# Kernel optimization log

Measured on AMD Instinct MI355X. Metric: run time of the kernel, lower is better.

The kernel has to match this reference:

```python
import jax, jax.numpy as jnp
import numpy as np

# ---- column/activation layout (matches transformer_info init kwarg) ----
N_COLS = 20          # continuous data columns
MODES = 50           # VGM modes per column (gumbel-softmax width)
SPAN = MODES + 1     # 1 tanh scalar + MODES gumbel logits
IN_DIM = 2048
OUT_DIM = N_COLS * SPAN  # 1020
TAU = 0.2
B = 16384
EPS = 1e-9

_spans = []
for i in range(N_COLS):
    st = i * SPAN
    _spans.append((st, st + 1, 0))          # tanh span (alpha)
    _spans.append((st + 1, st + SPAN, 1))   # gumbel-softmax span (beta/d)
N_SEG = len(_spans)

_seg = np.zeros(OUT_DIM, np.int32)   # segment id per output feature
_typ = np.zeros(OUT_DIM, np.int32)   # 0 = tanh, 1 = gumbel-softmax
for si, (s, e, t) in enumerate(_spans):
    _seg[s:e] = si
    _typ[s:e] = t
SEG = jnp.asarray(_seg)
TYP = jnp.asarray(_typ)


def setup_inputs() -> dict:
    key = jax.random.key(0)
    kx, kw, kb, ku = jax.random.split(key, 4)
    bound = 1.0 / np.sqrt(IN_DIM)  # init_bounded(dim=input_dim)
    x = jax.random.normal(kx, (B, IN_DIM), dtype=jnp.float32)
    W = jax.random.uniform(kw, (IN_DIM, OUT_DIM), minval=-bound, maxval=bound, dtype=jnp.float32)
    b = jax.random.uniform(kb, (OUT_DIM,), minval=-bound, maxval=bound, dtype=jnp.float32)
    u = jax.random.uniform(ku, (B, OUT_DIM), dtype=jnp.float32)  # uniform driving gumbel noise
    return {"x": x, "W": W, "b": b, "u": u}


def _segment_softmax(z):
    # softmax over each transformer_info span, fused via segment ops.
    zT = z.T  # [D, B]
    m = jax.ops.segment_max(zT, SEG, num_segments=N_SEG)      # [S, B]
    e = jnp.exp(zT - m[SEG])
    s = jax.ops.segment_sum(e, SEG, num_segments=N_SEG)       # [S, B]
    return (e / s[SEG]).T  # [B, D]


def reference(x, W, b, u):
    outputs = x @ W + b  # [B, OUT_DIM]
    # Gumbel(0,1) noise from uniform u
    g = -jnp.log(-jnp.log(jnp.clip(u, EPS, 1.0 - EPS)))
    soft = _segment_softmax((outputs + g) / TAU)
    # type 0 -> tanh, type 1 -> gumbel-softmax (single fused select)
    data_t = jnp.where(TYP == 0, jnp.tanh(outputs), soft)
    return outputs, data_t
```

## Files before the change

### kernel.cpp

```cpp
#include <hip/hip_runtime.h>
#include <stdint.h>

#define MDIM 16384
#define NDIM 1020
#define KDIM 2048
#define NPAD 1024
#define TK   (KDIM / 64)

typedef __attribute__((ext_vector_type(4))) float f32x4;
typedef __attribute__((ext_vector_type(8))) short short8;

#define MFMA16(a, b, c) __builtin_amdgcn_mfma_f32_16x16x32_bf16((a), (b), (c), 0, 0, 0)

template <int OFF>
static __device__ __forceinline__ short8 dsr(unsigned addr) {
    short8 r;
    asm volatile("ds_read_b128 %0, %1 offset:%2" : "=v"(r) : "v"(addr), "i"(OFF));
    return r;
}

#define LGKM(N)                                                       \
    asm volatile("s_waitcnt lgkmcnt(" #N ")" ::: "memory");           \
    __builtin_amdgcn_sched_barrier(0);

__device__ __forceinline__ unsigned short f2bf(float f) {
    unsigned int u = __float_as_uint(f);
    unsigned int r = (u + 0x7FFFu + ((u >> 16) & 1u)) >> 16;
    return (unsigned short)r;
}

__global__ void prep_w_kernel(const float* __restrict__ W,
                              unsigned short* __restrict__ Wt) {
    const int id = blockIdx.x * 256 + threadIdx.x;
    const int n0 = (id & 255) * 4;
    const int k0 = (id >> 8) * 4;
    float a[4][4];
    if (n0 < NDIM) {
#pragma unroll
        for (int i = 0; i < 4; ++i) {
            const float* p = W + (size_t)(k0 + i) * NDIM + n0;
            a[i][0] = p[0]; a[i][1] = p[1]; a[i][2] = p[2]; a[i][3] = p[3];
        }
    } else {
#pragma unroll
        for (int i = 0; i < 4; ++i)
#pragma unroll
            for (int j = 0; j < 4; ++j) a[i][j] = 0.f;
    }
#pragma unroll
    for (int j = 0; j < 4; ++j) {
        uint2 p;
        p.x = (unsigned)f2bf(a[0][j]) | ((unsigned)f2bf(a[1][j]) << 16);
        p.y = (unsigned)f2bf(a[2][j]) | ((unsigned)f2bf(a[3][j]) << 16);
        *(uint2*)(Wt + (size_t)(n0 + j) * KDIM + k0) = p;
    }
}

__global__ void prep_x_kernel(const float* __restrict__ x,
                              unsigned short* __restrict__ Xb) {
    const size_t total = (size_t)MDIM * KDIM;
    const size_t stride = (size_t)gridDim.x * 256 * 8;
    for (size_t i = ((size_t)blockIdx.x * 256 + threadIdx.x) * 8; i < total; i += stride) {
        const float4 v0 = *(const float4*)(x + i);
        const float4 v1 = *(const float4*)(x + i + 4);
        uint4 p;
        p.x = (unsigned)f2bf(v0.x) | ((unsigned)f2bf(v0.y) << 16);
        p.y = (unsigned)f2bf(v0.z) | ((unsigned)f2bf(v0.w) << 16);
        p.z = (unsigned)f2bf(v1.x) | ((unsigned)f2bf(v1.y) << 16);
        p.w = (unsigned)f2bf(v1.z) | ((unsigned)f2bf(v1.w) << 16);
        *(uint4*)(Xb + i) = p;
    }
}

extern "C" __global__ __launch_bounds__(512, 2) void gemm8_kernel(
    const unsigned short* __restrict__ Xb,
    const unsigned short* __restrict__ Wt,
    const float* __restrict__ bias,
    float* __restrict__ out) {
    extern __shared__ unsigned short lds_raw[];

    const int tid  = threadIdx.x;
    const int lane = tid & 63;
    const int wid  = tid >> 6;
    const int wr   = wid >> 2;
    const int wc   = wid & 3;

    const int bid = blockIdx.x;
    const int swz = (bid & 7) * 32 + (bid >> 3);
    const int bm  = swz >> 2;
    const int bn  = swz & 3;

    const int srow = wid * 8 + (lane >> 3);
    const int scb  = ((lane & 7) ^ (lane >> 3)) * 8;
    const unsigned short* aS = Xb + (size_t)(bm * 256 + srow) * KDIM + scb;
    const unsigned short* bS = Wt + (size_t)(bn * 256 + srow) * KDIM + scb;

#define STAGE(BUFI, OP, STRIPE, S) do {                                          \
    const size_t ks_ = (size_t)(((S) * 64) & (KDIM - 1));                        \
    const unsigned short* sp_ =                                                  \
        ((OP) ? bS : aS) + (size_t)((STRIPE) * 64) * KDIM + ks_;                 \
    __builtin_amdgcn_global_load_lds(                                            \
        (const __attribute__((address_space(1))) unsigned int*)sp_,              \
        (__attribute__((address_space(3))) unsigned int*)(lds_raw +              \
            (BUFI) * 32768 + (OP) * 16384 + ((STRIPE) * 64 + wid * 8) * 64),     \
        16, 0, 0);                                                              \
} while (0)

    const unsigned ldsbase =
        (unsigned)(uintptr_t)(__attribute__((address_space(3))) unsigned short*)lds_raw;
    const unsigned l15 = lane & 15, hi = lane >> 4, l7 = lane & 7;
    const unsigned c0 = (unsigned)((0 * 4 + hi) ^ l7) << 4;
    const unsigned c1 = (unsigned)((1 * 4 + hi) ^ l7) << 4;
    const unsigned pbA = ldsbase + (unsigned)(wr * 128 + l15) * 128;
    const unsigned pbB = ldsbase + 32768u + (unsigned)(wc * 64 + l15) * 128;
    const unsigned aA0_0 = pbA + c0,          aA0_1 = pbA + c1;
    const unsigned aA1_0 = pbA + 65536u + c0, aA1_1 = pbA + 65536u + c1;
    const unsigned bB0_0 = pbB + c0,          bB0_1 = pbB + c1;
    const unsigned bB1_0 = pbB + 65536u + c0, bB1_1 = pbB + 65536u + c1;

    f32x4 acc[8][4];
#pragma unroll
    for (int i = 0; i < 8; ++i)
#pragma unroll
        for (int j = 0; j < 4; ++j) {
            f32x4 z = {0.f, 0.f, 0.f, 0.f};
            acc[i][j] = z;
        }

    short8 af0[8], af1[8];
    short8 bfv[4][2];

#define RB(BUF, K)                                                    \
    bfv[0][K] = dsr<0 * 2048>(bB##BUF##_##K);                         \
    bfv[1][K] = dsr<1 * 2048>(bB##BUF##_##K);                         \
    bfv[2][K] = dsr<2 * 2048>(bB##BUF##_##K);                         \
    bfv[3][K] = dsr<3 * 2048>(bB##BUF##_##K);

#define RA(BUF, K, MF) af##K[MF] = dsr<(MF) * 2048>(aA##BUF##_##K);

#define G(K, MF, LG)                                                  \
    LGKM(LG)                                                          \
    __builtin_amdgcn_s_setprio(1);                                    \
    acc[MF][0] = MFMA16(af##K[MF], bfv[0][K], acc[MF][0]);            \
    acc[MF][1] = MFMA16(af##K[MF], bfv[1][K], acc[MF][1]);            \
    acc[MF][2] = MFMA16(af##K[MF], bfv[2][K], acc[MF][2]);            \
    acc[MF][3] = MFMA16(af##K[MF], bfv[3][K], acc[MF][3]);            \
    __builtin_amdgcn_s_setprio(0);

#define TILE(T, BUF)                                                            \
  {                                                                             \
    RB(BUF, 0)                                                  \
    RA(BUF, 0, 0) RA(BUF, 0, 1) RA(BUF, 0, 2) RA(BUF, 0, 3)                     \
    RA(BUF, 0, 4) RA(BUF, 0, 5) RA(BUF, 0, 6) RA(BUF, 0, 7)       \
    RB(BUF, 1)                                                  \
    G(0, 0, 11) G(0, 1, 10) G(0, 2, 9) G(0, 3, 8) G(0, 4, 7) G(0, 5, 6)         \
    RA(BUF, 1, 0) RA(BUF, 1, 1) RA(BUF, 1, 2) RA(BUF, 1, 3)                     \
    RA(BUF, 1, 4) RA(BUF, 1, 5) RA(BUF, 1, 6) RA(BUF, 1, 7)      \
    G(0, 6, 13) G(0, 7, 12)                                                     \
    G(1, 0, 7) G(1, 1, 6) G(1, 2, 5) G(1, 3, 4)                                 \
    G(1, 4, 3) G(1, 5, 2) G(1, 6, 1) G(1, 7, 0)                                 \
    __builtin_amdgcn_s_barrier();        \
    STAGE(BUF, 0, 0, (T) + 2); STAGE(BUF, 0, 1, (T) + 2);                       \
    STAGE(BUF, 0, 2, (T) + 2); STAGE(BUF, 0, 3, (T) + 2);                       \
    STAGE(BUF, 1, 0, (T) + 2); STAGE(BUF, 1, 1, (T) + 2);                       \
    STAGE(BUF, 1, 2, (T) + 2); STAGE(BUF, 1, 3, (T) + 2);                       \
    asm volatile("s_waitcnt vmcnt(8)" ::: "memory");      \
    __builtin_amdgcn_sched_barrier(0);                                          \
    __builtin_amdgcn_s_barrier();                                               \
  }

    STAGE(0, 0, 0, 0); STAGE(0, 0, 1, 0); STAGE(0, 0, 2, 0); STAGE(0, 0, 3, 0);
    STAGE(0, 1, 0, 0); STAGE(0, 1, 1, 0); STAGE(0, 1, 2, 0); STAGE(0, 1, 3, 0);
    STAGE(1, 0, 0, 1); STAGE(1, 0, 1, 1); STAGE(1, 0, 2, 1); STAGE(1, 0, 3, 1);
    STAGE(1, 1, 0, 1); STAGE(1, 1, 1, 1); STAGE(1, 1, 2, 1); STAGE(1, 1, 3, 1);
    asm volatile("s_waitcnt vmcnt(8)" ::: "memory");
    __builtin_amdgcn_sched_barrier(0);
    __builtin_amdgcn_s_barrier();

    for (int t2 = 0; t2 < TK; t2 += 2) {
        TILE(t2, 0)
        TILE(t2 + 1, 1)
    }

#pragma unroll
    for (int nf = 0; nf < 4; ++nf) {
        const int col = bn * 256 + wc * 64 + nf * 16 + (lane & 15);
        if (col < NDIM) {
            const float bv = bias[col];
#pragma unroll
            for (int mf = 0; mf < 8; ++mf) {
                const int row = bm * 256 + wr * 128 + mf * 16 + ((lane >> 4) << 2);
                float* op = out + (size_t)row * NDIM + col;
#pragma unroll
                for (int r = 0; r < 4; ++r)
                    op[(size_t)r * NDIM] = acc[mf][nf][r] + bv;
            }
        }
    }
#undef STAGE
#undef RB
#undef RA
#undef G
#undef TILE
}

__global__ void gemm_bf_kernel(const unsigned short* __restrict__ Xb,
                               const unsigned short* __restrict__ Wt,
                               const float* __restrict__ bias,
                               float* __restrict__ out) {
    __shared__ __align__(16) unsigned short As[128][32];
    __shared__ __align__(16) unsigned short Bs[128][32];

    const int tid  = threadIdx.x;
    const int lane = tid & 63;
    const int wid  = tid >> 6;
    const int wr   = wid >> 1;
    const int wc   = wid & 1;
    const int bn   = blockIdx.x;
    const int bm   = blockIdx.y;

    f32x4 acc[4][4];
#pragma unroll
    for (int i = 0; i < 4; ++i)
#pragma unroll
        for (int j = 0; j < 4; ++j) {
            f32x4 z = {0.f, 0.f, 0.f, 0.f};
            acc[i][j] = z;
        }

    const unsigned short* abase =
        Xb + (size_t)(bm * 128 + wid * 16 + (lane >> 2)) * KDIM + (lane & 3) * 8;
    const unsigned short* bbase =
        Wt + (size_t)(bn * 128 + wid * 16 + (lane >> 2)) * KDIM + (lane & 3) * 8;

    for (int kt = 0; kt < KDIM; kt += 32) {
#pragma unroll
        for (int j = 0; j < 2; ++j)
            __builtin_amdgcn_global_load_lds(
                (const __attribute__((address_space(1))) unsigned int*)(abase + (size_t)j * 64 * KDIM + kt),
                (__attribute__((address_space(3))) unsigned int*)(&As[j * 64 + wid * 16][0]),
                16, 0, 0);
#pragma unroll
        for (int j = 0; j < 2; ++j)
            __builtin_amdgcn_global_load_lds(
                (const __attribute__((address_space(1))) unsigned int*)(bbase + (size_t)j * 64 * KDIM + kt),
                (__attribute__((address_space(3))) unsigned int*)(&Bs[j * 64 + wid * 16][0]),
                16, 0, 0);
        __syncthreads();

        short8 af[4], bfr[4];
#pragma unroll
        for (int mi = 0; mi < 4; ++mi)
            af[mi] = *(const short8*)&As[wr * 64 + mi * 16 + (lane & 15)][(lane >> 4) * 8];
#pragma unroll
        for (int ni = 0; ni < 4; ++ni)
            bfr[ni] = *(const short8*)&Bs[wc * 64 + ni * 16 + (lane & 15)][(lane >> 4) * 8];

#pragma unroll
        for (int mi = 0; mi < 4; ++mi)
#pragma unroll
            for (int ni = 0; ni < 4; ++ni)
                acc[mi][ni] = MFMA16(af[mi], bfr[ni], acc[mi][ni]);

        __syncthreads();
    }

#pragma unroll
    for (int ni = 0; ni < 4; ++ni) {
        const int col = bn * 128 + wc * 64 + ni * 16 + (lane & 15);
        if (col < NDIM) {
            const float bv = bias[col];
#pragma unroll
            for (int mi = 0; mi < 4; ++mi) {
                const int row = bm * 128 + wr * 64 + mi * 16 + ((lane >> 4) << 2);
                float* op = out + (size_t)row * NDIM + col;
#pragma unroll
                for (int r = 0; r < 4; ++r)
                    op[(size_t)r * NDIM] = acc[mi][ni][r] + bv;
            }
        }
    }
}

__global__ void act_kernel(const float* __restrict__ outp,
                           const float* __restrict__ u,
                           float* __restrict__ dt) {
    const int lane  = threadIdx.x & 63;
    const int gwave = (blockIdx.x * 256 + threadIdx.x) >> 6;
    const int nwave = gridDim.x * 4;
    const int total = MDIM * 20;
    const float NEG_INF = -__builtin_inff();

    for (int unit = gwave; unit < total; unit += nwave) {
        const int row = unit / 20;
        const int sp  = unit - row * 20;
        const size_t base = (size_t)row * NDIM + sp * 51;

        float o = 0.f, uu = 0.5f;
        if (lane < 51) {
            o  = outp[base + lane];
            uu = u[base + lane];
        }
        const bool soft = (lane >= 1) && (lane < 51);

        const float uc = fmaxf(uu, 1e-9f);
        const float g  = -__logf(-__logf(uc));
        float z = soft ? (o + g) * 5.0f : NEG_INF;

        float m = z;
#pragma unroll
        for (int off = 32; off; off >>= 1) m = fmaxf(m, __shfl_xor(m, off));
        float e = soft ? __expf(z - m) : 0.f;
        float s = e;
#pragma unroll
        for (int off = 32; off; off >>= 1) s += __shfl_xor(s, off);

        float res;
        if (lane == 0) {
            const float ex = __expf(-2.0f * fabsf(o));
            const float t  = (1.0f - ex) / (1.0f + ex);
            res = copysignf(t, o);
        } else {
            res = e / s;
        }
        if (lane < 51) dt[base + lane] = res;
    }
}

extern "C" void kernel_launch(void* const* d_in, const int* in_sizes, int n_in,
                              void* d_out, int out_size, void* d_ws, size_t ws_size,
                              hipStream_t stream) {
    const float* x = (const float*)d_in[0];
    const float* W = (const float*)d_in[1];
    const float* b = (const float*)d_in[2];
    const float* u = (const float*)d_in[3];
    float* out = (float*)d_out;
    float* dt  = out + (size_t)MDIM * NDIM;
    unsigned short* Wt = (unsigned short*)d_ws;
    unsigned short* Xb = Wt + (size_t)NPAD * KDIM;

    prep_w_kernel<<<512, 256, 0, stream>>>(W, Wt);
    prep_x_kernel<<<2048, 256, 0, stream>>>(x, Xb);

    const hipError_t attr_ok = hipFuncSetAttribute(
        (const void*)gemm8_kernel, hipFuncAttributeMaxDynamicSharedMemorySize, 131072);
    if (attr_ok == hipSuccess) {
        gemm8_kernel<<<256, 512, 131072, stream>>>(Xb, Wt, b, out);
    } else {
        gemm_bf_kernel<<<dim3(8, 128), 256, 0, stream>>>(Xb, Wt, b, out);
    }

    act_kernel<<<8192, 256, 0, stream>>>(out, u, dt);
}
```

Measured before the change: 194.6 us.

## Load B fragments directly from global into registers, halve LDS staging

The GEMM kernel stops staging the W tile through LDS. Each wave now loads its B fragments straight from global memory into double-buffered registers, one tile ahead, while A stays LDS-staged with a two-tile double buffer of 64KB. The pipeline depth drops from two tiles in flight to one, with a full vmcnt(0) wait each tile. This removes LDS traffic and bank pressure for B, but each wave in a block re-reads B from global or L2 without LDS reuse, adds register pressure, and exposes more memory latency per iteration.

Measured after the change: 228.2 us. 1.17x slower.

```diff
diff --git a/kernel.cpp b/kernel.cpp
--- a/kernel.cpp
+++ b/kernel.cpp
@@ -72,7 +72,7 @@
     }
 }
 
-extern "C" __global__ __launch_bounds__(512, 2) void gemm8_kernel(
+extern "C" __global__ __launch_bounds__(512, 2) void gemm9_kernel(
     const unsigned short* __restrict__ Xb,
     const unsigned short* __restrict__ Wt,
     const float* __restrict__ bias,
@@ -93,17 +93,15 @@
     const int srow = wid * 8 + (lane >> 3);
     const int scb  = ((lane & 7) ^ (lane >> 3)) * 8;
     const unsigned short* aS = Xb + (size_t)(bm * 256 + srow) * KDIM + scb;
-    const unsigned short* bS = Wt + (size_t)(bn * 256 + srow) * KDIM + scb;
-
-#define STAGE(BUFI, OP, STRIPE, S) do {                                          \
-    const size_t ks_ = (size_t)(((S) * 64) & (KDIM - 1));                        \
+
+#define STAGEA(BUFI, STRIPE, S) do {                                             \
     const unsigned short* sp_ =                                                  \
-        ((OP) ? bS : aS) + (size_t)((STRIPE) * 64) * KDIM + ks_;                 \
+        aS + (size_t)((STRIPE) * 64) * KDIM + (size_t)(((S) & 31) * 64);         \
     __builtin_amdgcn_global_load_lds(                                            \
         (const __attribute__((address_space(1))) unsigned int*)sp_,              \
         (__attribute__((address_space(3))) unsigned int*)(lds_raw +              \
-            (BUFI) * 32768 + (OP) * 16384 + ((STRIPE) * 64 + wid * 8) * 64),     \
-        16, 0, 0);                                                              \
+            (BUFI) * 16384 + ((STRIPE) * 64 + wid * 8) * 64),                    \
+        16, 0, 0);                                                               \
 } while (0)
 
     const unsigned ldsbase =
@@ -112,11 +110,23 @@
     const unsigned c0 = (unsigned)((0 * 4 + hi) ^ l7) << 4;
     const unsigned c1 = (unsigned)((1 * 4 + hi) ^ l7) << 4;
     const unsigned pbA = ldsbase + (unsigned)(wr * 128 + l15) * 128;
-    const unsigned pbB = ldsbase + 32768u + (unsigned)(wc * 64 + l15) * 128;
     const unsigned aA0_0 = pbA + c0,          aA0_1 = pbA + c1;
-    const unsigned aA1_0 = pbA + 65536u + c0, aA1_1 = pbA + 65536u + c1;
-    const unsigned bB0_0 = pbB + c0,          bB0_1 = pbB + c1;
-    const unsigned bB1_0 = pbB + 65536u + c0, bB1_1 = pbB + 65536u + c1;
+    const unsigned aA1_0 = pbA + 32768u + c0, aA1_1 = pbA + 32768u + c1;
+
+    const unsigned short* bsrc =
+        Wt + (size_t)(bn * 256 + wc * 64 + l15) * KDIM + hi * 8;
+
+#define LOADB(DST, T) {                                                   \
+    const unsigned short* bp_ = bsrc + (size_t)(((T) & 31)) * 64;         \
+    DST[0][0] = *(const short8*)(bp_);                                    \
+    DST[0][1] = *(const short8*)(bp_ + 32);                               \
+    DST[1][0] = *(const short8*)(bp_ + 16 * KDIM);                        \
+    DST[1][1] = *(const short8*)(bp_ + 16 * KDIM + 32);                   \
+    DST[2][0] = *(const short8*)(bp_ + 32 * KDIM);                        \
+    DST[2][1] = *(const short8*)(bp_ + 32 * KDIM + 32);                   \
+    DST[3][0] = *(const short8*)(bp_ + 48 * KDIM);                        \
+    DST[3][1] = *(const short8*)(bp_ + 48 * KDIM + 32);                   \
+}
 
     f32x4 acc[8][4];
 #pragma unroll
@@ -127,59 +137,53 @@
             acc[i][j] = z;
         }
 
-    short8 af0[8], af1[8];
-    short8 bfv[4][2];
-
-#define RB(BUF, K)                                                    \
-    bfv[0][K] = dsr<0 * 2048>(bB##BUF##_##K);                         \
-    bfv[1][K] = dsr<1 * 2048>(bB##BUF##_##K);                         \
-    bfv[2][K] = dsr<2 * 2048>(bB##BUF##_##K);                         \
-    bfv[3][K] = dsr<3 * 2048>(bB##BUF##_##K);
-
-#define RA(BUF, K, MF) af##K[MF] = dsr<(MF) * 2048>(aA##BUF##_##K);
-
-#define G(K, MF, LG)                                                  \
+    short8 bP[4][2], bQ[4][2];
+
+#define G4(MF, AF, KH, BC, LG)                                        \
     LGKM(LG)                                                          \
-    __builtin_amdgcn_s_setprio(1);                                    \
-    acc[MF][0] = MFMA16(af##K[MF], bfv[0][K], acc[MF][0]);            \
-    acc[MF][1] = MFMA16(af##K[MF], bfv[1][K], acc[MF][1]);            \
-    acc[MF][2] = MFMA16(af##K[MF], bfv[2][K], acc[MF][2]);            \
-    acc[MF][3] = MFMA16(af##K[MF], bfv[3][K], acc[MF][3]);            \
-    __builtin_amdgcn_s_setprio(0);
-
-#define TILE(T, BUF)                                                            \
+    acc[MF][0] = MFMA16(AF, BC[0][KH], acc[MF][0]);                   \
+    acc[MF][1] = MFMA16(AF, BC[1][KH], acc[MF][1]);                   \
+    acc[MF][2] = MFMA16(AF, BC[2][KH], acc[MF][2]);                   \
+    acc[MF][3] = MFMA16(AF, BC[3][KH], acc[MF][3]);
+
+#define TILE(T, BUF, NB, BCUR, BNXT)                                            \
   {                                                                             \
-    RB(BUF, 0)                                                  \
-    RA(BUF, 0, 0) RA(BUF, 0, 1) RA(BUF, 0, 2) RA(BUF, 0, 3)                     \
-    RA(BUF, 0, 4) RA(BUF, 0, 5) RA(BUF, 0, 6) RA(BUF, 0, 7)       \
-    RB(BUF, 1)                                                  \
-    G(0, 0, 11) G(0, 1, 10) G(0, 2, 9) G(0, 3, 8) G(0, 4, 7) G(0, 5, 6)         \
-    RA(BUF, 1, 0) RA(BUF, 1, 1) RA(BUF, 1, 2) RA(BUF, 1, 3)                     \
-    RA(BUF, 1, 4) RA(BUF, 1, 5) RA(BUF, 1, 6) RA(BUF, 1, 7)      \
-    G(0, 6, 13) G(0, 7, 12)                                                     \
-    G(1, 0, 7) G(1, 1, 6) G(1, 2, 5) G(1, 3, 4)                                 \
-    G(1, 4, 3) G(1, 5, 2) G(1, 6, 1) G(1, 7, 0)                                 \
-    __builtin_amdgcn_s_barrier();        \
-    STAGE(BUF, 0, 0, (T) + 2); STAGE(BUF, 0, 1, (T) + 2);                       \
-    STAGE(BUF, 0, 2, (T) + 2); STAGE(BUF, 0, 3, (T) + 2);                       \
-    STAGE(BUF, 1, 0, (T) + 2); STAGE(BUF, 1, 1, (T) + 2);                       \
-    STAGE(BUF, 1, 2, (T) + 2); STAGE(BUF, 1, 3, (T) + 2);                       \
-    asm volatile("s_waitcnt vmcnt(8)" ::: "memory");      \
+    STAGEA(NB, 0, (T) + 1); STAGEA(NB, 1, (T) + 1);                             \
+    STAGEA(NB, 2, (T) + 1); STAGEA(NB, 3, (T) + 1);                             \
+    LOADB(BNXT, (T) + 1)                                                        \
+    __builtin_amdgcn_sched_barrier(0);                                          \
+    __builtin_amdgcn_s_setprio(1);                                              \
+    short8 x0 = dsr<0>(aA##BUF##_0),     x1 = dsr<2048>(aA##BUF##_0);           \
+    short8 x2 = dsr<4096>(aA##BUF##_0),  x3 = dsr<6144>(aA##BUF##_0);           \
+    short8 x4 = dsr<8192>(aA##BUF##_0),  x5 = dsr<10240>(aA##BUF##_0);          \
+    short8 x6 = dsr<12288>(aA##BUF##_0), x7 = dsr<14336>(aA##BUF##_0);          \
+    G4(0, x0, 0, BCUR, 7) G4(1, x1, 0, BCUR, 6)                                 \
+    G4(2, x2, 0, BCUR, 5) G4(3, x3, 0, BCUR, 4)                                 \
+    short8 y0 = dsr<0>(aA##BUF##_1),     y1 = dsr<2048>(aA##BUF##_1);           \
+    short8 y2 = dsr<4096>(aA##BUF##_1),  y3 = dsr<6144>(aA##BUF##_1);           \
+    G4(4, x4, 0, BCUR, 7) G4(5, x5, 0, BCUR, 6)                                 \
+    G4(6, x6, 0, BCUR, 5) G4(7, x7, 0, BCUR, 4)                                 \
+    short8 y4 = dsr<8192>(aA##BUF##_1),  y5 = dsr<10240>(aA##BUF##_1);          \
+    short8 y6 = dsr<12288>(aA##BUF##_1), y7 = dsr<14336>(aA##BUF##_1);          \
+    G4(0, y0, 1, BCUR, 7) G4(1, y1, 1, BCUR, 6)                                 \
+    G4(2, y2, 1, BCUR, 5) G4(3, y3, 1, BCUR, 4)                                 \
+    G4(4, y4, 1, BCUR, 3) G4(5, y5, 1, BCUR, 2)                                 \
+    G4(6, y6, 1, BCUR, 1) G4(7, y7, 1, BCUR, 0)                                 \
+    __builtin_amdgcn_s_setprio(0);                                              \
+    asm volatile("s_waitcnt vmcnt(0)" ::: "memory");                            \
     __builtin_amdgcn_sched_barrier(0);                                          \
     __builtin_amdgcn_s_barrier();                                               \
   }
 
-    STAGE(0, 0, 0, 0); STAGE(0, 0, 1, 0); STAGE(0, 0, 2, 0); STAGE(0, 0, 3, 0);
-    STAGE(0, 1, 0, 0); STAGE(0, 1, 1, 0); STAGE(0, 1, 2, 0); STAGE(0, 1, 3, 0);
-    STAGE(1, 0, 0, 1); STAGE(1, 0, 1, 1); STAGE(1, 0, 2, 1); STAGE(1, 0, 3, 1);
-    STAGE(1, 1, 0, 1); STAGE(1, 1, 1, 1); STAGE(1, 1, 2, 1); STAGE(1, 1, 3, 1);
-    asm volatile("s_waitcnt vmcnt(8)" ::: "memory");
+    STAGEA(0, 0, 0); STAGEA(0, 1, 0); STAGEA(0, 2, 0); STAGEA(0, 3, 0);
+    LOADB(bP, 0)
+    asm volatile("s_waitcnt vmcnt(0)" ::: "memory");
     __builtin_amdgcn_sched_barrier(0);
     __builtin_amdgcn_s_barrier();
 
     for (int t2 = 0; t2 < TK; t2 += 2) {
-        TILE(t2, 0)
-        TILE(t2 + 1, 1)
+        TILE(t2,     0, 1, bP, bQ)
+        TILE(t2 + 1, 1, 0, bQ, bP)
     }
 
 #pragma unroll
@@ -197,10 +201,9 @@
             }
         }
     }
-#undef STAGE
-#undef RB
-#undef RA
-#undef G
+#undef STAGEA
+#undef LOADB
+#undef G4
 #undef TILE
 }
 
@@ -343,9 +346,9 @@
     prep_x_kernel<<<2048, 256, 0, stream>>>(x, Xb);
 
     const hipError_t attr_ok = hipFuncSetAttribute(
-        (const void*)gemm8_kernel, hipFuncAttributeMaxDynamicSharedMemorySize, 131072);
+        (const void*)gemm9_kernel, hipFuncAttributeMaxDynamicSharedMemorySize, 65536);
     if (attr_ok == hipSuccess) {
-        gemm8_kernel<<<256, 512, 131072, stream>>>(Xb, Wt, b, out);
+        gemm9_kernel<<<256, 512, 65536, stream>>>(Xb, Wt, b, out);
     } else {
         gemm_bf_kernel<<<dim3(8, 128), 256, 0, stream>>>(Xb, Wt, b, out);
     }
```
